# Performance work log

Measured on AMD Instinct MI355X. Metric: run time of the kernel, lower is better.

## Reference

```python
import jax, jax.numpy as jnp
import numpy as np
from jax import lax

CHUNK = 256
ROPE_BASE = 10000.0


def setup_inputs() -> dict:
    D, H, K = 2048, 16, 4
    Dh = D // H
    key = jax.random.key(0)
    ks = jax.random.split(key, 8)
    x = jax.random.normal(ks[0], (2, 4096, D), dtype=jnp.float32)
    norm_scale = jnp.ones((D,), jnp.float32)
    conv_w = jax.random.normal(ks[1], (D, 1, K), jnp.float32) * 0.1
    conv_b = jnp.zeros((D,), jnp.float32)
    in_proj_w = jax.random.normal(ks[2], (3 * D, D), jnp.float32) * 0.02
    out_proj_w = jax.random.normal(ks[3], (D, D), jnp.float32) * 0.02
    # dt_bias init as in torch module
    u = jax.random.uniform(ks[4], (H, Dh), jnp.float32)
    dt = jnp.clip(jnp.exp(u * (np.log(0.1) - np.log(10.0)) + np.log(10.0)), 0.001, None)
    dt_bias = (dt + jnp.log(-jnp.expm1(-dt))).reshape(-1)
    head_mix = jnp.eye(H, dtype=jnp.float32)
    return {"x": x, "norm_scale": norm_scale, "conv_w": conv_w, "conv_b": conv_b,
            "in_proj_w": in_proj_w, "dt_bias": dt_bias, "head_mix": head_mix,
            "out_proj_w": out_proj_w}


def _forward(x, norm_scale, conv_w, conv_b, in_proj_w, dt_bias, head_mix, out_proj_w):
    B, N, D = x.shape
    H = head_mix.shape[0]
    Dh = D // H
    K = conv_w.shape[-1]
    residual = x
    # RMSNorm (fp32 with clamp)
    xf = x.astype(jnp.float32)
    rms = lax.rsqrt(jnp.mean(xf * xf, -1, keepdims=True) + 1e-6)
    xn = jnp.clip(norm_scale * xf * rms, -60000.0, 60000.0).astype(x.dtype)
    # causal depthwise conv1d (torch pads K-1 then truncates to N)
    xc = lax.conv_general_dilated(xn.transpose(0, 2, 1), conv_w, (1,), [(K - 1, 0)],
                                  dimension_numbers=("NCH", "OIH", "NCH"),
                                  feature_group_count=D)
    xc = xc + conv_b[None, :, None]
    xc = jax.nn.silu(xc.transpose(0, 2, 1))  # (B,N,D)
    fused = xc @ in_proj_w.T  # (B,N,3D)
    dt_raw, v, gate = jnp.split(fused, 3, axis=-1)
    dt = jnp.clip(jax.nn.softplus(dt_raw.astype(jnp.float32) + dt_bias), 0.001, 2.0)
    gate = jax.nn.sigmoid(gate)
    log_alpha = -dt  # (B,N,D) fp32
    # RoPE on v per head
    inv_freq = 1.0 / (ROPE_BASE ** (jnp.arange(0, Dh, 2, dtype=jnp.float32) / Dh))
    t = jnp.arange(N, dtype=jnp.float32)
    freqs = t[:, None] * inv_freq[None, :]  # (N, Dh//2)
    cos = jnp.cos(freqs)[None, :, None, :]
    sin = jnp.sin(freqs)[None, :, None, :]
    v4 = v.reshape(B, N, H, Dh)
    v1, v2 = v4[..., : Dh // 2], v4[..., Dh // 2:]
    v_rot = jnp.concatenate([v1 * cos - v2 * sin, v1 * sin + v2 * cos], -1).reshape(B, N, D)
    v_in = v_rot * dt  # fp32
    # pad to chunk multiple (static)
    pad = (-N) % CHUNK
    if pad:
        v_in = jnp.pad(v_in, ((0, 0), (0, pad), (0, 0)))
        log_alpha = jnp.pad(log_alpha, ((0, 0), (0, pad), (0, 0)))
    NC = v_in.shape[1] // CHUNK
    vc = v_in.reshape(B, NC, CHUNK, D)
    la = log_alpha.reshape(B, NC, CHUNK, D)
    # intra-chunk stabilized scan
    L = jnp.clip(jnp.cumsum(la, axis=2), -20.0, 0.0)
    Lmax = jnp.max(L, axis=2, keepdims=True)
    Ls = L - Lmax
    cum = jnp.cumsum(jnp.exp(-Ls) * vc, axis=2)
    chunk_out = jnp.exp(Ls) * cum
    if NC > 1:
        bd = L[:, :, -1, :]             # (B,NC,D) boundary decay
        bo = chunk_out[:, :, -1, :]     # boundary out
        cd = jnp.clip(jnp.cumsum(bd, axis=1), -80.0, 0.0)
        stab = jnp.max(cd, axis=1, keepdims=True)
        ncd = jnp.clip(cd - stab, -20.0, 0.0)
        seeds = bo * jnp.exp(-ncd)
        shifted = jnp.pad(seeds[:, :-1], ((0, 0), (1, 0), (0, 0)))
        carries = jnp.cumsum(shifted, axis=1) * jnp.exp(ncd)
        final = chunk_out + carries[:, :, None, :] * jnp.exp(L)
    else:
        final = chunk_out
    final = final.astype(x.dtype).reshape(B, -1, D)[:, :N, :]
    # head mixing
    vm = jnp.einsum("bnhd,hm->bnmd", final.reshape(B, N, H, Dh), head_mix).reshape(B, N, D)
    out = (vm * gate) @ out_proj_w.T
    return residual + out


def reference(x, norm_scale, conv_w, conv_b, in_proj_w, dt_bias, head_mix, out_proj_w):
    return _forward(x, norm_scale, conv_w, conv_b, in_proj_w, dt_bias, head_mix, out_proj_w)
```

## Files before the change

### kernel.cpp

```cpp
#include <hip/hip_runtime.h>
#include <hip/hip_bf16.h>
#include <math.h>

#define B_ 2
#define N_ 4096
#define D_ 2048
#define H_ 16
#define DH_ 128
#define CHUNK_ 256
#define NC_ 16
#define M_ (B_*N_)
#define F3D (3*D_)

typedef __bf16 v8bf __attribute__((ext_vector_type(8)));
typedef float  v4f  __attribute__((ext_vector_type(4)));
typedef unsigned short u16x8 __attribute__((ext_vector_type(8)));

__device__ __forceinline__ float bf2f(unsigned short u) {
    union { unsigned int i; float f; } c; c.i = ((unsigned int)u) << 16; return c.f;
}
__device__ __forceinline__ unsigned short f2bf(float f) {
    __hip_bfloat16 h = __float2bfloat16(f);
    return *(unsigned short*)&h;
}

__device__ __forceinline__ void async_copy16(void* lds, const void* g) {
    __builtin_amdgcn_global_load_lds(
        (const __attribute__((address_space(1))) unsigned int*)g,
        (__attribute__((address_space(3))) unsigned int*)lds,
        16, 0, 0);
}

__global__ __launch_bounds__(256) void k_rmsnorm(const float* __restrict__ x,
                                                 const float* __restrict__ scale,
                                                 __hip_bfloat16* __restrict__ xn)
{
    __shared__ float red[4];
    const int row = blockIdx.x;
    const float4* x4 = (const float4*)(x + (size_t)row * D_);
    float4 a = x4[threadIdx.x*2];
    float4 b = x4[threadIdx.x*2 + 1];
    float ss = a.x*a.x + a.y*a.y + a.z*a.z + a.w*a.w
             + b.x*b.x + b.y*b.y + b.z*b.z + b.w*b.w;
    #pragma unroll
    for (int off = 32; off > 0; off >>= 1) ss += __shfl_down(ss, off, 64);
    if ((threadIdx.x & 63) == 0) red[threadIdx.x >> 6] = ss;
    __syncthreads();
    float tot = red[0] + red[1] + red[2] + red[3];
    float r = rsqrtf(tot / (float)D_ + 1e-6f);
    const float4* s4 = (const float4*)scale;
    float4 sa = s4[threadIdx.x*2];
    float4 sb = s4[threadIdx.x*2 + 1];
    float v[8] = { sa.x*a.x, sa.y*a.y, sa.z*a.z, sa.w*a.w,
                   sb.x*b.x, sb.y*b.y, sb.z*b.z, sb.w*b.w };
    u16x8 o;
    #pragma unroll
    for (int j = 0; j < 8; ++j) {
        float t = fminf(fmaxf(v[j]*r, -60000.f), 60000.f);
        o[j] = f2bf(t);
    }
    ((u16x8*)(xn + (size_t)row * D_))[threadIdx.x] = o;
}

__global__ __launch_bounds__(256) void k_conv_silu(const __hip_bfloat16* __restrict__ xn,
                                                   const float* __restrict__ w,
                                                   const float* __restrict__ bias,
                                                   __hip_bfloat16* __restrict__ xc)
{
    size_t p = (size_t)blockIdx.x * 256 + threadIdx.x;
    size_t e0 = p * 8;
    int d0 = (int)(e0 & (D_-1));
    int n  = (int)((e0 >> 11) & (N_-1));
    const float4* w4 = (const float4*)w;
    float acc[8];
    const float4* b4 = (const float4*)(bias + d0);
    float4 ba = b4[0], bb = b4[1];
    acc[0]=ba.x; acc[1]=ba.y; acc[2]=ba.z; acc[3]=ba.w;
    acc[4]=bb.x; acc[5]=bb.y; acc[6]=bb.z; acc[7]=bb.w;
    float4 wv[8];
    #pragma unroll
    for (int j = 0; j < 8; ++j) wv[j] = w4[d0 + j];
    #pragma unroll
    for (int k = 0; k < 4; ++k) {
        int nn = n - 3 + k;
        if (nn >= 0) {
            u16x8 t = *(const u16x8*)(xn + e0 - (size_t)(3-k)*D_);
            #pragma unroll
            for (int j = 0; j < 8; ++j) {
                float wk = (k==0)?wv[j].x:(k==1)?wv[j].y:(k==2)?wv[j].z:wv[j].w;
                acc[j] += bf2f(t[j]) * wk;
            }
        }
    }
    u16x8 o;
    #pragma unroll
    for (int j = 0; j < 8; ++j) {
        float s = acc[j] / (1.f + __expf(-acc[j]));
        o[j] = f2bf(s);
    }
    *(u16x8*)(xc + e0) = o;
}

__global__ __launch_bounds__(256) void k_cast_bf16(const float* __restrict__ src,
                                                   __hip_bfloat16* __restrict__ dst)
{
    size_t p = (size_t)blockIdx.x * 256 + threadIdx.x;
    const float4* s4 = (const float4*)src;
    float4 a = s4[p*2], b = s4[p*2 + 1];
    u16x8 o;
    o[0]=f2bf(a.x); o[1]=f2bf(a.y); o[2]=f2bf(a.z); o[3]=f2bf(a.w);
    o[4]=f2bf(b.x); o[5]=f2bf(b.y); o[6]=f2bf(b.z); o[7]=f2bf(b.w);
    ((u16x8*)dst)[p] = o;
}

template<int MODE>
__global__ __launch_bounds__(512, 2) void k_gemm(const __hip_bfloat16* __restrict__ Abf,
                                              const __hip_bfloat16* __restrict__ Wbf,
                                              int K,
                                              float* __restrict__ o0,
                                              __hip_bfloat16* __restrict__ o1,
                                              __hip_bfloat16* __restrict__ o2,
                                              const float* __restrict__ dt_bias,
                                              const float* __restrict__ resid,
                                              float* __restrict__ outp)
{
    __shared__ __attribute__((aligned(16))) char lds[3][2][16384];
    const __bf16* A = (const __bf16*)Abf;
    const __bf16* W = (const __bf16*)Wbf;
    const int tid  = threadIdx.x;
    const int wave = tid >> 6;
    const int lane = tid & 63;

    const int gx  = gridDim.x;
    int bid = blockIdx.y * gx + blockIdx.x;
    int cpx = (gx * gridDim.y) >> 3;
    int swzb = (bid & 7) * cpx + (bid >> 3);
    int bx = swzb % gx, by = swzb / gx;

    const size_t m0 = (size_t)bx * 256;
    const size_t n0 = (size_t)by * 256;
    const int wm = (wave & 1) * 128;
    const int wn = (wave >> 1) * 64;

    v4f acc[8][4] = {};

    const int fr = lane & 15;
    const int qk = lane >> 4;
    const int colb = ((qk ^ ((fr >> 1) & 3)) << 4);
    int rowA[8], rowB[4];
    #pragma unroll
    for (int i = 0; i < 8; ++i) rowA[i] = (wm + i*16 + fr) * 64;
    #pragma unroll
    for (int j = 0; j < 4; ++j) rowB[j] = (wn + j*16 + fr) * 64;

    const int rowi   = tid >> 2;
    const int col16s = tid & 3;
    const int scol   = (col16s ^ ((rowi >> 1) & 3)) * 8;

    const int nt = K >> 5;

    auto stage = [&](int t, int half, int isB) {
        char* dst = lds[t % 3][isB] + (half * 8192 + wave * 1024);
        int rfull = half * 128 + rowi;
        size_t grow = (isB ? n0 : m0) + (size_t)rfull;
        const __bf16* src = (isB ? W : A) + grow * (size_t)K + (t << 5) + scol;
        async_copy16((void*)dst, (const void*)src);
    };

    #pragma unroll
    for (int h = 0; h < 2; ++h) { stage(0, h, 0); stage(0, h, 1); }
    #pragma unroll
    for (int h = 0; h < 2; ++h) { stage(1, h, 0); stage(1, h, 1); }

    for (int t = 0; t < nt; ++t) {
        if (t + 1 < nt) { asm volatile("s_waitcnt vmcnt(4)" ::: "memory"); }
        else            { asm volatile("s_waitcnt vmcnt(0)" ::: "memory"); }
        __builtin_amdgcn_s_barrier();
        __builtin_amdgcn_sched_barrier(0);

        const char* Ab = lds[t % 3][0];
        const char* Bb = lds[t % 3][1];

        if (t + 2 < nt) {
            stage(t + 2, 0, 0); stage(t + 2, 1, 0);
            stage(t + 2, 0, 1); stage(t + 2, 1, 1);
        }

        v8bf fa[8], fb[4];
        #pragma unroll
        for (int j = 0; j < 4; ++j) fb[j] = *(const v8bf*)(Bb + rowB[j] + colb);
        #pragma unroll
        for (int i = 0; i < 8; ++i) fa[i] = *(const v8bf*)(Ab + rowA[i] + colb);

        __builtin_amdgcn_s_setprio(1);
        #pragma unroll
        for (int i = 0; i < 8; ++i)
            #pragma unroll
            for (int j = 0; j < 4; ++j)
                acc[i][j] = __builtin_amdgcn_mfma_f32_16x16x32_bf16(fa[i], fb[j], acc[i][j], 0, 0, 0);
        __builtin_amdgcn_s_setprio(0);
    }

    const int col = lane & 15;
    const int rb  = (lane >> 4) * 4;
    if (MODE == 0) {
        const int stream = by >> 3;
        const size_t nb = n0 - (size_t)stream * D_;
        #pragma unroll
        for (int i = 0; i < 8; ++i)
            #pragma unroll
            for (int j = 0; j < 4; ++j) {
                size_t nIdx = nb + wn + j*16 + col;
                #pragma unroll
                for (int r = 0; r < 4; ++r) {
                    size_t m = m0 + wm + i*16 + rb + r;
                    size_t off = m * (size_t)D_ + nIdx;
                    float v = acc[i][j][r];
                    if (stream == 0) {
                        float xx = v + dt_bias[nIdx];
                        float e  = __expf(-fabsf(xx));
                        float sp = fmaxf(xx, 0.f) + __logf(1.f + e);
                        float dt = fminf(fmaxf(sp, 0.001f), 2.0f);
                        o0[off] = -dt;
                    } else if (stream == 1) {
                        o1[off] = __float2bfloat16(v);
                    } else {
                        o2[off] = __float2bfloat16(1.f/(1.f+__expf(-v)));
                    }
                }
            }
    } else {
        #pragma unroll
        for (int i = 0; i < 8; ++i)
            #pragma unroll
            for (int j = 0; j < 4; ++j)
                #pragma unroll
                for (int r = 0; r < 4; ++r) {
                    size_t m = m0 + wm + i*16 + rb + r;
                    size_t off = m * (size_t)D_ + n0 + wn + j*16 + col;
                    outp[off] = acc[i][j][r] + resid[off];
                }
    }
}

__global__ __launch_bounds__(256) void k_scan1(const float* __restrict__ la,
                                               const __hip_bfloat16* __restrict__ v,
                                               float* __restrict__ bd, float* __restrict__ bo)
{
    int idx = blockIdx.x * 256 + threadIdx.x;
    int d = idx & (D_-1);
    int c = (idx >> 11) & (NC_-1);
    int b = idx >> 15;
    int i = d & 63;
    const bool firstHalf = (d & 64) == 0;
    float inv = __expf((float)i * (-9.210340371976184f / 64.f));
    int n0 = c * CHUNK_;
    float cs = cosf((float)n0 * inv), sn = sinf((float)n0 * inv);
    float ca = cosf(inv), sa = sinf(inv);
    size_t row0 = (size_t)b * N_ + (size_t)c * CHUNK_;
    float S = 0.f, Lp = 0.f, out = 0.f;
    #pragma unroll 8
    for (int t = 0; t < CHUNK_; ++t) {
        size_t off = (row0 + t) * (size_t)D_ + d;
        float a  = la[off];
        float vo = __bfloat162float(v[off]);
        float vp = __bfloat162float(v[firstHalf ? off + 64 : off - 64]);
        float dt = -a;
        float vin = (firstHalf ? (vo*cs - vp*sn) : (vp*sn + vo*cs)) * dt;
        S += a;
        float L = fmaxf(S, -20.f);
        out = __expf(L - Lp) * out + vin;
        Lp = L;
        float csn = cs*ca - sn*sa;
        sn = sn*ca + cs*sa;
        cs = csn;
    }
    bd[idx] = Lp;
    bo[idx] = out;
}

__global__ __launch_bounds__(256) void k_scan2(const float* __restrict__ bd,
                                               const float* __restrict__ bo,
                                               float* __restrict__ carries)
{
    int idx = blockIdx.x * 256 + threadIdx.x;
    int d = idx & (D_-1);
    int b = idx >> 11;
    float bd0 = bd[(size_t)(b*NC_)*D_ + d];
    float cd = 0.f, acc = 0.f;
    #pragma unroll
    for (int c = 0; c < NC_; ++c) {
        size_t o = (size_t)(b*NC_ + c)*D_ + d;
        cd = fmaxf(cd + bd[o], -80.f);
        float ncd = fmaxf(cd - bd0, -20.f);
        carries[o] = acc * __expf(ncd);
        acc += bo[o] * __expf(-ncd);
    }
}

__global__ __launch_bounds__(256) void k_scan3(const float* __restrict__ la,
                                               const __hip_bfloat16* __restrict__ v,
                                               const float* __restrict__ carries,
                                               __hip_bfloat16* __restrict__ state)
{
    int idx = blockIdx.x * 256 + threadIdx.x;
    int d = idx & (D_-1);
    int c = (idx >> 11) & (NC_-1);
    int b = idx >> 15;
    int i = d & 63;
    const bool firstHalf = (d & 64) == 0;
    float inv = __expf((float)i * (-9.210340371976184f / 64.f));
    int n0 = c * CHUNK_;
    float cs = cosf((float)n0 * inv), sn = sinf((float)n0 * inv);
    float ca = cosf(inv), sa = sinf(inv);
    float carry = carries[idx];
    size_t row0 = (size_t)b * N_ + (size_t)c * CHUNK_;
    float S = 0.f, Lp = 0.f, out = 0.f;
    #pragma unroll 8
    for (int t = 0; t < CHUNK_; ++t) {
        size_t off = (row0 + t) * (size_t)D_ + d;
        float a  = la[off];
        float vo = __bfloat162float(v[off]);
        float vp = __bfloat162float(v[firstHalf ? off + 64 : off - 64]);
        float dt = -a;
        float vin = (firstHalf ? (vo*cs - vp*sn) : (vp*sn + vo*cs)) * dt;
        S += a;
        float L = fmaxf(S, -20.f);
        out = __expf(L - Lp) * out + vin;
        Lp = L;
        state[off] = __float2bfloat16(out + carry * __expf(L));
        float csn = cs*ca - sn*sa;
        sn = sn*ca + cs*sa;
        cs = csn;
    }
}

__global__ __launch_bounds__(256) void k_headmix_gate(const __hip_bfloat16* __restrict__ state,
                                                      const __hip_bfloat16* __restrict__ gate,
                                                      const float* __restrict__ hm,
                                                      __hip_bfloat16* __restrict__ y)
{
    __shared__ float lf[D_];
    __shared__ float lhm[H_*H_];
    const int row = blockIdx.x;
    const size_t base = (size_t)row * D_;
    u16x8 s8 = ((const u16x8*)(state + base))[threadIdx.x];
    #pragma unroll
    for (int j = 0; j < 8; ++j) lf[threadIdx.x*8 + j] = bf2f(s8[j]);
    if (threadIdx.x < H_*H_) lhm[threadIdx.x] = hm[threadIdx.x];
    __syncthreads();
    #pragma unroll
    for (int k = 0; k < 8; ++k) {
        int o = threadIdx.x + k*256;
        int m  = o >> 7;
        int dh = o & 127;
        float s = 0.f;
        #pragma unroll
        for (int h = 0; h < H_; ++h) s += lf[h*DH_ + dh] * lhm[h*H_ + m];
        float g = __bfloat162float(gate[base + o]);
        y[base + o] = __float2bfloat16(s * g);
    }
}

extern "C" void kernel_launch(void* const* d_in, const int* in_sizes, int n_in,
                              void* d_out, int out_size, void* d_ws, size_t ws_size,
                              hipStream_t stream)
{
    const float* x          = (const float*)d_in[0];
    const float* norm_scale = (const float*)d_in[1];
    const float* conv_w     = (const float*)d_in[2];
    const float* conv_b     = (const float*)d_in[3];
    const float* in_proj_w  = (const float*)d_in[4];
    const float* dt_bias    = (const float*)d_in[5];
    const float* head_mix   = (const float*)d_in[6];
    const float* out_proj_w = (const float*)d_in[7];
    float* out = (float*)d_out;

    char* ws = (char*)d_ws;
    float*          la   = (float*)ws;
    __hip_bfloat16* xn   = (__hip_bfloat16*)(ws + 67108864);
    __hip_bfloat16* xc   = (__hip_bfloat16*)(ws + 100663296);
    __hip_bfloat16* gate = (__hip_bfloat16*)(ws + 134217728);
    __hip_bfloat16* w2   = (__hip_bfloat16*)(ws + 167772160);
    float*          bd   = (float*)(ws + 176160768);
    float*          bo   = (float*)(ws + 176422912);
    float*          carr = (float*)(ws + 176685056);
    __hip_bfloat16* w1   = xn;
    __hip_bfloat16* y    = xc;
    __hip_bfloat16* v     = (__hip_bfloat16*)d_out;
    __hip_bfloat16* state = (__hip_bfloat16*)((char*)d_out + 33554432);

    k_rmsnorm<<<M_, 256, 0, stream>>>(x, norm_scale, xn);
    k_conv_silu<<<(M_*(size_t)D_)/8/256, 256, 0, stream>>>(xn, conv_w, conv_b, xc);
    k_cast_bf16<<<6144, 256, 0, stream>>>(in_proj_w, w1);
    k_cast_bf16<<<2048, 256, 0, stream>>>(out_proj_w, w2);
    k_gemm<0><<<dim3(M_/256, F3D/256), 512, 0, stream>>>(xc, w1, D_, la, v, gate, dt_bias, nullptr, nullptr);
    k_scan1<<<(B_*NC_*D_)/256, 256, 0, stream>>>(la, v, bd, bo);
    k_scan2<<<(B_*D_)/256, 256, 0, stream>>>(bd, bo, carr);
    k_scan3<<<(B_*NC_*D_)/256, 256, 0, stream>>>(la, v, carr, state);
    k_headmix_gate<<<M_, 256, 0, stream>>>(state, gate, head_mix, y);
    k_gemm<1><<<dim3(M_/256, D_/256), 512, 0, stream>>>(y, w2, D_, nullptr, nullptr, nullptr, nullptr, x, out);
}
```

Measured before the change: 713.2 us.

## Restructure GEMM main loop into 8-phase ping-pong schedule with BK=64 tiles

Replaces the triple-buffered BK=32 GEMM loop with a double-buffered BK=64 scheme. Each K-tile is split into four quadrant phases that interleave LDS fragment reads, async global-to-LDS staging of the next tile halves, and MFMA blocks, with barriers around each phase. The LDS swizzle is changed to an 8-way XOR for 128-byte rows. The goal is better overlap of memory traffic with matrix math and fewer LDS bank conflicts. In exchange it adds many more barriers per iteration, and staging clamps out-of-range tiles, which issues redundant loads near the end of the loop.

```diff
diff --git a/kernel.cpp b/kernel.cpp
--- a/kernel.cpp
+++ b/kernel.cpp
@@ -30,6 +30,11 @@
         (__attribute__((address_space(3))) unsigned int*)lds,
         16, 0, 0);
 }
+
+#define BAR_LG() do { __builtin_amdgcn_s_barrier(); \
+                      asm volatile("s_waitcnt lgkmcnt(0)" ::: "memory"); } while(0)
+#define ENDBAR() __builtin_amdgcn_s_barrier()
+#define VM4()    asm volatile("s_waitcnt vmcnt(4)" ::: "memory")
 
 __global__ __launch_bounds__(256) void k_rmsnorm(const float* __restrict__ x,
                                                  const float* __restrict__ scale,
@@ -124,7 +129,7 @@
                                               const float* __restrict__ resid,
                                               float* __restrict__ outp)
 {
-    __shared__ __attribute__((aligned(16))) char lds[3][2][16384];
+    __shared__ __attribute__((aligned(16))) char lds[2][2][32768];
     const __bf16* A = (const __bf16*)Abf;
     const __bf16* W = (const __bf16*)Wbf;
     const int tid  = threadIdx.x;
@@ -146,60 +151,93 @@
 
     const int fr = lane & 15;
     const int qk = lane >> 4;
-    const int colb = ((qk ^ ((fr >> 1) & 3)) << 4);
-    int rowA[8], rowB[4];
-    #pragma unroll
-    for (int i = 0; i < 8; ++i) rowA[i] = (wm + i*16 + fr) * 64;
-    #pragma unroll
-    for (int j = 0; j < 4; ++j) rowB[j] = (wn + j*16 + fr) * 64;
-
-    const int rowi   = tid >> 2;
-    const int col16s = tid & 3;
-    const int scol   = (col16s ^ ((rowi >> 1) & 3)) * 8;
-
-    const int nt = K >> 5;
-
-    auto stage = [&](int t, int half, int isB) {
-        char* dst = lds[t % 3][isB] + (half * 8192 + wave * 1024);
-        int rfull = half * 128 + rowi;
-        size_t grow = (isB ? n0 : m0) + (size_t)rfull;
-        const __bf16* src = (isB ? W : A) + grow * (size_t)K + (t << 5) + scol;
-        async_copy16((void*)dst, (const void*)src);
+    const int sw0 = ((0 + qk) ^ (fr & 7)) << 4;
+    const int sw1 = ((4 + qk) ^ (fr & 7)) << 4;
+
+    const int srow = lane >> 3;
+    const int scol = ((lane & 7) ^ srow) * 8;
+
+    const int NT = K >> 6;
+
+    auto stage = [&](int T, int isB, int h) {
+        const int Tc = T < NT ? T : NT - 1;
+        char* base = &lds[T & 1][isB][0] + h * 16384 + wave * 1024;
+        const __bf16* gp = (isB ? W + n0 * (size_t)K : A + m0 * (size_t)K);
+        #pragma unroll
+        for (int q = 0; q < 2; ++q) {
+            const __bf16* src = gp + (size_t)(h*128 + q*64 + wave*8 + srow) * K
+                                   + (Tc << 6) + scol;
+            async_copy16((void*)(base + q * 8192), (const void*)src);
+        }
     };
-
-    #pragma unroll
-    for (int h = 0; h < 2; ++h) { stage(0, h, 0); stage(0, h, 1); }
-    #pragma unroll
-    for (int h = 0; h < 2; ++h) { stage(1, h, 0); stage(1, h, 1); }
-
-    for (int t = 0; t < nt; ++t) {
-        if (t + 1 < nt) { asm volatile("s_waitcnt vmcnt(4)" ::: "memory"); }
-        else            { asm volatile("s_waitcnt vmcnt(0)" ::: "memory"); }
-        __builtin_amdgcn_s_barrier();
-        __builtin_amdgcn_sched_barrier(0);
-
-        const char* Ab = lds[t % 3][0];
-        const char* Bb = lds[t % 3][1];
-
-        if (t + 2 < nt) {
-            stage(t + 2, 0, 0); stage(t + 2, 1, 0);
-            stage(t + 2, 0, 1); stage(t + 2, 1, 1);
+    auto rdA = [&](v8bf* f, const char* bufA, int mh) {
+        #pragma unroll
+        for (int i = 0; i < 4; ++i) {
+            const int row = (wm + mh*64 + i*16 + fr) * 128;
+            f[i*2+0] = *(const v8bf*)(bufA + row + sw0);
+            f[i*2+1] = *(const v8bf*)(bufA + row + sw1);
         }
-
-        v8bf fa[8], fb[4];
-        #pragma unroll
-        for (int j = 0; j < 4; ++j) fb[j] = *(const v8bf*)(Bb + rowB[j] + colb);
-        #pragma unroll
-        for (int i = 0; i < 8; ++i) fa[i] = *(const v8bf*)(Ab + rowA[i] + colb);
-
+    };
+    auto rdB = [&](v8bf* f, const char* bufB, int nh) {
+        #pragma unroll
+        for (int g = 0; g < 2; ++g) {
+            const int row = (wn + nh*32 + g*16 + fr) * 128;
+            f[g*2+0] = *(const v8bf*)(bufB + row + sw0);
+            f[g*2+1] = *(const v8bf*)(bufB + row + sw1);
+        }
+    };
+    auto mma = [&](int mh, int nh, const v8bf* fa, const v8bf* fb) {
         __builtin_amdgcn_s_setprio(1);
         #pragma unroll
-        for (int i = 0; i < 8; ++i)
+        for (int ks = 0; ks < 2; ++ks)
             #pragma unroll
-            for (int j = 0; j < 4; ++j)
-                acc[i][j] = __builtin_amdgcn_mfma_f32_16x16x32_bf16(fa[i], fb[j], acc[i][j], 0, 0, 0);
+            for (int i = 0; i < 4; ++i)
+                #pragma unroll
+                for (int g = 0; g < 2; ++g)
+                    acc[mh*4+i][nh*2+g] = __builtin_amdgcn_mfma_f32_16x16x32_bf16(
+                        fa[i*2+ks], fb[g*2+ks], acc[mh*4+i][nh*2+g], 0, 0, 0);
         __builtin_amdgcn_s_setprio(0);
-    }
+    };
+
+    stage(0, 0, 0); stage(0, 0, 1); stage(0, 1, 0); stage(0, 1, 1);
+    stage(1, 0, 0); stage(1, 0, 1);
+    VM4();
+    __builtin_amdgcn_s_barrier();
+
+    const char* Ac = &lds[0][0][0];
+    const char* Bc = &lds[0][1][0];
+    const char* Ad = &lds[1][0][0];
+    const char* Bd = &lds[1][1][0];
+
+    for (int i2 = 0; i2 < (NT >> 1); ++i2) {
+        const int t = i2 * 2;
+        v8bf fa0[8], fa1[8], fb0[4], fb1[4];
+        rdA(fa0, Ac, 0); rdB(fb0, Bc, 0);
+        stage(t+1, 1, 0);
+        BAR_LG(); mma(0, 0, fa0, fb0); ENDBAR();
+        rdA(fa1, Ac, 1);
+        stage(t+1, 1, 1);
+        BAR_LG(); mma(1, 0, fa1, fb0); ENDBAR();
+        rdB(fb1, Bc, 1);
+        stage(t+2, 0, 0);
+        BAR_LG(); mma(0, 1, fa0, fb1); ENDBAR();
+        stage(t+2, 0, 1);
+        VM4();
+        BAR_LG(); mma(1, 1, fa1, fb1); ENDBAR();
+        rdA(fa0, Ad, 0); rdB(fb0, Bd, 0);
+        stage(t+2, 1, 0);
+        BAR_LG(); mma(0, 0, fa0, fb0); ENDBAR();
+        rdA(fa1, Ad, 1);
+        stage(t+2, 1, 1);
+        BAR_LG(); mma(1, 0, fa1, fb0); ENDBAR();
+        rdB(fb1, Bd, 1);
+        stage(t+3, 0, 0);
+        BAR_LG(); mma(0, 1, fa0, fb1); ENDBAR();
+        stage(t+3, 0, 1);
+        VM4();
+        BAR_LG(); mma(1, 1, fa1, fb1); ENDBAR();
+    }
+    asm volatile("s_waitcnt vmcnt(0)" ::: "memory");
 
     const int col = lane & 15;
     const int rb  = (lane >> 4) * 4;
```

Measured after the change: 724.3 us. No clear change (+1.5%).
